# Kernel tuning notes

Measured on AMD Instinct MI355X. Metric: run time of the kernel, lower is better.

## Reference

```python
import jax, jax.numpy as jnp
from jax import lax
import numpy as np

# Dims matching init_kwargs
V = 32000      # vocab
D = 768        # d_model
L = 4          # n_layers
N = 16         # state_size
K = 4          # conv kernel
I = 2 * D      # intermediate = expand * d_model = 1536
DT = (D + 15) // 16  # time_step_rank = 48
BATCH, SEQ = 4, 2048
EPS = 1e-5


def setup_inputs() -> dict:
    key = jax.random.key(0)
    ks = jax.random.split(key, 12)
    s = 0.02
    A_init = jnp.broadcast_to(jnp.arange(1, N + 1, dtype=jnp.float32), (L, I, N))
    return {
        "input_ids": jax.random.randint(ks[0], (BATCH, SEQ), 0, V, dtype=jnp.int32),
        "embed": jax.random.normal(ks[1], (V, D), jnp.float32) * s,        # tied lm_head
        "norm_w": jnp.ones((L, D), jnp.float32),
        "in_proj_w": jax.random.normal(ks[2], (L, 2 * I, D), jnp.float32) * s,
        "conv_w": jax.random.normal(ks[3], (L, I, K), jnp.float32) * s,
        "conv_b": jnp.zeros((L, I), jnp.float32),
        "x_proj_w": jax.random.normal(ks[4], (L, DT + 2 * N, I), jnp.float32) * s,
        "dt_proj_w": jax.random.normal(ks[5], (L, I, DT), jnp.float32) * s,
        "dt_proj_b": jax.random.normal(ks[6], (L, I), jnp.float32) * s,
        "A_log": jnp.log(A_init),
        "D_param": jnp.ones((L, I), jnp.float32),
        "out_proj_w": jax.random.normal(ks[7], (L, D, I), jnp.float32) * s,
        "norm_f_w": jnp.ones((D,), jnp.float32),
    }


def rmsnorm(x, w):
    return x * lax.rsqrt(jnp.mean(x * x, axis=-1, keepdims=True) + EPS) * w


def mamba_mixer(x, in_w, cw, cb, xp_w, dtp_w, dtp_b, a_log, d_par, out_w):
    # x: [B, S, D]
    proj = jnp.einsum('bsd,ed->bse', x, in_w)            # [B, S, 2I]
    u, gate = jnp.split(proj, 2, axis=-1)                # each [B, S, I]
    # causal depthwise conv1d (HF pads K-1 then truncates to S == left pad)
    uc = u.transpose(0, 2, 1)                            # [B, I, S]
    conv = lax.conv_general_dilated(
        uc, cw[:, None, :], window_strides=(1,), padding=[(K - 1, 0)],
        feature_group_count=I, dimension_numbers=('NCH', 'OIH', 'NCH'))
    ut = jax.nn.silu(conv + cb[None, :, None]).transpose(0, 2, 1)  # [B, S, I]
    # SSM parameters
    xdbl = jnp.einsum('bsi,ei->bse', ut, xp_w)           # [B, S, DT+2N]
    dt_r = xdbl[..., :DT]
    Bm = xdbl[..., DT:DT + N]                            # [B, S, N]
    Cm = xdbl[..., DT + N:]                              # [B, S, N]
    dt = jax.nn.softplus(jnp.einsum('bsr,ir->bsi', dt_r, dtp_w) + dtp_b)  # [B, S, I]
    A = -jnp.exp(a_log)                                  # [I, N]

    def step(h, ins):
        dt_t, B_t, C_t, u_t = ins                        # [B,I],[B,N],[B,N],[B,I]
        dA = jnp.exp(dt_t[..., None] * A)                # [B, I, N]
        h = dA * h + (dt_t[..., None] * B_t[:, None, :]) * u_t[..., None]
        y = jnp.einsum('bin,bn->bi', h, C_t)
        return h, y

    h0 = jnp.zeros((x.shape[0], I, N), x.dtype)
    xs = (dt.transpose(1, 0, 2), Bm.transpose(1, 0, 2),
          Cm.transpose(1, 0, 2), ut.transpose(1, 0, 2))
    _, ys = lax.scan(step, h0, xs)                       # [S, B, I]
    y = ys.transpose(1, 0, 2) + ut * d_par               # skip D term
    y = y * jax.nn.silu(gate)
    return jnp.einsum('bsi,di->bsd', y, out_w)           # [B, S, D]


def reference(input_ids, embed, norm_w, in_proj_w, conv_w, conv_b, x_proj_w,
              dt_proj_w, dt_proj_b, A_log, D_param, out_proj_w, norm_f_w):
    h = embed[input_ids]                                 # [B, S, D]
    for l in range(L):
        h = h + mamba_mixer(rmsnorm(h, norm_w[l]), in_proj_w[l], conv_w[l],
                            conv_b[l], x_proj_w[l], dt_proj_w[l], dt_proj_b[l],
                            A_log[l], D_param[l], out_proj_w[l])
    h = rmsnorm(h, norm_f_w)
    # module returns logits[:, -1]; compute only last-token logits (tied lm_head)
    return h[:, -1] @ embed.T                            # [B, V]
```

## Files before the change

kernel.cpp:

```cpp
#include <hip/hip_runtime.h>
#include <hip/hip_bf16.h>

#define Vv 32000
#define Dm 768
#define Lm 4
#define Nst 16
#define Kc 4
#define Im 1536
#define DTr 48
#define Bt 4
#define Sq 2048
#define TOK (Bt*Sq)
#define EPSf 1e-5f
#define NC 64
#define CL 32
#define QROWS (Bt*NC*16)
#define LOG2E 1.4426950408889634f
#define LN2f  0.6931471805599453f

using bf16 = __hip_bfloat16;
typedef __bf16 bf16x8 __attribute__((ext_vector_type(8)));
typedef float f32x4 __attribute__((ext_vector_type(4)));

__device__ __forceinline__ float b2f(bf16 x){ return __bfloat162float(x); }
__device__ __forceinline__ bf16 f2b(float x){ return __float2bfloat16(x); }
__device__ __forceinline__ float us2f(ushort u){ unsigned x = (unsigned)u << 16; return __builtin_bit_cast(float, x); }

__device__ __forceinline__ float ex2(float x){
#if __has_builtin(__builtin_amdgcn_exp2f)
  return __builtin_amdgcn_exp2f(x);
#else
  float r; asm("v_exp_f32 %0, %1" : "=v"(r) : "v"(x)); return r;
#endif
}
__device__ __forceinline__ float vlog2(float x){
#if __has_builtin(__builtin_amdgcn_logf)
  return __builtin_amdgcn_logf(x);
#else
  float r; asm("v_log_f32 %0, %1" : "=v"(r) : "v"(x)); return r;
#endif
}
__device__ __forceinline__ float frcp(float x){
#if __has_builtin(__builtin_amdgcn_rcpf)
  return __builtin_amdgcn_rcpf(x);
#else
  float r; asm("v_rcp_f32 %0, %1" : "=v"(r) : "v"(x)); return r;
#endif
}

#define GLDS(gp, lp) __builtin_amdgcn_global_load_lds( \
    (const __attribute__((address_space(1))) void*)(gp), \
    (__attribute__((address_space(3))) void*)(lp), 16, 0, 0)

__global__ __launch_bounds__(256) void k_cvt(const float* __restrict__ src,
                                             bf16* __restrict__ dst, int n){
  int i = (blockIdx.x*256 + threadIdx.x)*4;
  if (i >= n) return;
  float4 v = *(const float4*)(src + i);
  bf16* o = dst + i;
  o[0]=f2b(v.x); o[1]=f2b(v.y); o[2]=f2b(v.z); o[3]=f2b(v.w);
}

__global__ __launch_bounds__(256) void k_cvt_xpw(const float* __restrict__ src,
                                                 bf16* __restrict__ dst){
  int idx = blockIdx.x*256 + threadIdx.x;
  int l = idx / (128*Im); int rem = idx - l*128*Im;
  int r = rem / Im;       int c = rem - r*Im;
  dst[idx] = (r < 80) ? f2b(src[((size_t)l*80 + r)*Im + c]) : f2b(0.f);
}

__global__ __launch_bounds__(256) void k_cvt_dtw(const float* __restrict__ src,
                                                 bf16* __restrict__ dst){
  int idx = blockIdx.x*256 + threadIdx.x;
  int l = idx / (Im*64); int rem = idx - l*Im*64;
  int r = rem / 64;      int c = rem - r*64;
  dst[idx] = (c < 48) ? f2b(src[((size_t)l*Im + r)*48 + c]) : f2b(0.f);
}

__global__ __launch_bounds__(256) void k_embed(const int* __restrict__ ids,
                                               const float* __restrict__ emb,
                                               float* __restrict__ h){
  int t = blockIdx.x;
  const float4* e = (const float4*)(emb + (size_t)ids[t]*Dm);
  float4* o = (float4*)(h + (size_t)t*Dm);
  if (threadIdx.x < Dm/4) o[threadIdx.x] = e[threadIdx.x];
}

__global__ __launch_bounds__(256) void k_rmsnorm(const float* __restrict__ h,
                                                 const float* __restrict__ w,
                                                 bf16* __restrict__ xb){
  int t = blockIdx.x;
  const float* x = h + (size_t)t*Dm;
  float v[3]; float ss = 0.f;
  #pragma unroll
  for (int j=0;j<3;j++){ v[j] = x[threadIdx.x + j*256]; ss += v[j]*v[j]; }
  #pragma unroll
  for (int off=32; off; off>>=1) ss += __shfl_xor(ss, off);
  __shared__ float sred[4];
  int wave = threadIdx.x>>6, lane = threadIdx.x&63;
  if (lane==0) sred[wave]=ss;
  __syncthreads();
  float tot = sred[0]+sred[1]+sred[2]+sred[3];
  float scale = rsqrtf(tot*(1.f/Dm) + EPSf);
  bf16* o = xb + (size_t)t*Dm;
  #pragma unroll
  for (int j=0;j<3;j++){ int d = threadIdx.x + j*256; o[d] = f2b(v[j]*scale*w[d]); }
}

__global__ __launch_bounds__(256) void k_rms_last(const float* __restrict__ h,
                                                  const float* __restrict__ w,
                                                  float* __restrict__ xf){
  int b = blockIdx.x;
  const float* x = h + ((size_t)b*Sq + (Sq-1))*Dm;
  float v[3]; float ss = 0.f;
  #pragma unroll
  for (int j=0;j<3;j++){ v[j] = x[threadIdx.x + j*256]; ss += v[j]*v[j]; }
  #pragma unroll
  for (int off=32; off; off>>=1) ss += __shfl_xor(ss, off);
  __shared__ float sred[4];
  int wave = threadIdx.x>>6, lane = threadIdx.x&63;
  if (lane==0) sred[wave]=ss;
  __syncthreads();
  float tot = sred[0]+sred[1]+sred[2]+sred[3];
  float scale = rsqrtf(tot*(1.f/Dm) + EPSf);
  float* o = xf + (size_t)b*Dm;
  #pragma unroll
  for (int j=0;j<3;j++){ int d = threadIdx.x + j*256; o[d] = v[j]*scale*w[d]; }
}

template<int MODE>
__global__ __launch_bounds__(256) void k_gemm(const bf16* __restrict__ A,
                                              const bf16* __restrict__ Bw,
                                              void* __restrict__ Cout,
                                              const float* __restrict__ bias,
                                              int M, int N, int K,
                                              int lda, int ldb, int ldc){
  __shared__ __align__(16) ushort Ash[128*32];
  __shared__ __align__(16) ushort Bsh[128*32];
  int tid = threadIdx.x;
  int bm = blockIdx.y, bn = blockIdx.x;
  int wave = tid >> 6, lane = tid & 63;
  int wrow = wave >> 1, wcol = wave & 1;
  int quad = lane >> 4, lq = lane & 15;

  f32x4 acc[4][4];
  #pragma unroll
  for (int a=0;a<4;a++)
    #pragma unroll
    for (int b=0;b<4;b++) acc[a][b] = (f32x4){0.f,0.f,0.f,0.f};

  const ushort* Ag = (const ushort*)A;
  const ushort* Bg = (const ushort*)Bw;

  for (int k0 = 0; k0 < K; k0 += 32) {
    __syncthreads();
    #pragma unroll
    for (int c = tid; c < 512; c += 256) {
      int row = c >> 2, col = (c & 3) * 8;
      GLDS(&Ag[(size_t)(bm*128 + row)*lda + k0 + col], &Ash[c*8]);
      GLDS(&Bg[(size_t)(bn*128 + row)*ldb + k0 + col], &Bsh[c*8]);
    }
    __syncthreads();
    bf16x8 af[4], bfr[4];
    #pragma unroll
    for (int a=0;a<4;a++){
      int m = wrow*64 + a*16 + lq;
      af[a] = __builtin_bit_cast(bf16x8, *(const uint4*)&Ash[m*32 + quad*8]);
    }
    #pragma unroll
    for (int b=0;b<4;b++){
      int n = wcol*64 + b*16 + lq;
      bfr[b] = __builtin_bit_cast(bf16x8, *(const uint4*)&Bsh[n*32 + quad*8]);
    }
    #pragma unroll
    for (int a=0;a<4;a++)
      #pragma unroll
      for (int b=0;b<4;b++)
        acc[a][b] = __builtin_amdgcn_mfma_f32_16x16x32_bf16(af[a], bfr[b], acc[a][b], 0, 0, 0);
  }
  #pragma unroll
  for (int a=0;a<4;a++)
    #pragma unroll
    for (int b=0;b<4;b++)
      #pragma unroll
      for (int r=0;r<4;r++){
        int row = bm*128 + wrow*64 + a*16 + quad*4 + r;
        int col = bn*128 + wcol*64 + b*16 + lq;
        size_t idx = (size_t)row*ldc + col;
        if (MODE == 0) ((bf16*)Cout)[idx] = f2b(acc[a][b][r]);
        else if (MODE == 1) ((float*)Cout)[idx] += acc[a][b][r];
        else {
          float v = acc[a][b][r] + bias[col];
          float sp;
          if (v > 20.f) sp = v;
          else { float e = ex2(v*LOG2E); sp = vlog2(1.f + e)*LN2f; }
          ((bf16*)Cout)[idx] = f2b(sp);
        }
      }
}

#define SA256(qm,k0s,bf_) { GLDS(Ag + sA[qm][0] + (k0s), lds + (bf_)*32768 + lA[qm][0]); \
                            GLDS(Ag + sA[qm][1] + (k0s), lds + (bf_)*32768 + lA[qm][1]); }
#define SB256(qn,k0s,bf_) { GLDS(Bg + sB[qn][0] + (k0s), lds + 65536 + (bf_)*32768 + lB[qn][0]); \
                            GLDS(Bg + sB[qn][1] + (k0s), lds + 65536 + (bf_)*32768 + lB[qn][1]); }
#define RD_A(qm_) do{ _Pragma("unroll") for(int m2=0;m2<4;m2++){ \
    int r = wm*128 + ((qm_)*4+m2)*16 + lq; \
    _Pragma("unroll") for(int kh=0;kh<2;kh++) \
      bA[m2][kh] = *(const uint4*)(Ab + (r<<7) + ((kh*64 + quad*16) ^ ((r&7)<<4))); } }while(0)
#define RD_B(qn_) do{ _Pragma("unroll") for(int n2=0;n2<2;n2++){ \
    int r = wn*64 + ((qn_)*2+n2)*16 + lq; \
    _Pragma("unroll") for(int kh=0;kh<2;kh++) \
      bB[qn_][n2][kh] = *(const uint4*)(Bb + (r<<7) + ((kh*64 + quad*16) ^ ((r&7)<<4))); } }while(0)
#define MMA256(qm_,qn_) do{ \
  __builtin_amdgcn_s_barrier(); \
  __builtin_amdgcn_sched_barrier(0); \
  __builtin_amdgcn_s_setprio(1); \
  _Pragma("unroll") for(int m2=0;m2<4;m2++) \
    _Pragma("unroll") for(int n2=0;n2<2;n2++) \
      _Pragma("unroll") for(int kh=0;kh<2;kh++) \
        acc[(qm_)*4+m2][(qn_)*2+n2] = __builtin_amdgcn_mfma_f32_16x16x32_bf16( \
          __builtin_bit_cast(bf16x8, bA[m2][kh]), __builtin_bit_cast(bf16x8, bB[qn_][n2][kh]), \
          acc[(qm_)*4+m2][(qn_)*2+n2], 0, 0, 0); \
  __builtin_amdgcn_s_setprio(0); \
  __builtin_amdgcn_s_barrier(); \
  __builtin_amdgcn_sched_barrier(0); \
}while(0)
#define VMW4 asm volatile("s_waitcnt vmcnt(4)":::"memory")

template<int MODE>
__global__ __launch_bounds__(512, 2) void k_gemm256(const bf16* __restrict__ A,
                                                    const bf16* __restrict__ Bw,
                                                    void* __restrict__ Cout,
                                                    int M, int N, int K,
                                                    int lda, int ldb, int ldc){
  __shared__ __align__(16) char lds[131072];
  int tid = threadIdx.x;
  int wave = tid >> 6, lane = tid & 63;
  int wm = wave >> 2, wn = wave & 3;
  int quad = lane >> 4, lq = lane & 15;
  int nx = gridDim.x;
  int nwg = nx * gridDim.y;
  int lin = blockIdx.y * nx + blockIdx.x;
  if ((nwg & 7) == 0){
    int cpx = nwg >> 3;
    lin = (lin & 7)*cpx + (lin >> 3);
  }
  int bm = lin / nx, bn = lin - bm*nx;
  const ushort* Ag = (const ushort*)A;
  const ushort* Bg = (const ushort*)Bw;

  size_t sA[2][2]; int lA[2][2];
  size_t sB[2][2]; int lB[2][2];
  #pragma unroll
  for (int qm=0; qm<2; qm++)
    #pragma unroll
    for (int d=0; d<2; d++){
      int r = d*128 + qm*64 + (tid>>3);
      int cb = ((tid&7)<<4) ^ ((r&7)<<4);
      sA[qm][d] = (size_t)(bm*256 + r)*lda + (cb>>1);
      lA[qm][d] = ((d*128 + qm*64)<<7) + tid*16;
    }
  #pragma unroll
  for (int qn=0; qn<2; qn++)
    #pragma unroll
    for (int d=0; d<2; d++){
      int g = 2*d + (wave>>2);
      int jj = tid & 255;
      int r = g*64 + qn*32 + (jj>>3);
      int cb = ((jj&7)<<4) ^ ((r&7)<<4);
      sB[qn][d] = (size_t)(bn*256 + r)*ldb + (cb>>1);
      lB[qn][d] = ((g*64 + qn*32)<<7) + jj*16;
    }

  f32x4 acc[8][4];
  #pragma unroll
  for (int a=0;a<8;a++)
    #pragma unroll
    for (int b=0;b<4;b++) acc[a][b] = (f32x4){0.f,0.f,0.f,0.f};

  SA256(0, 0, 0); SB256(0, 0, 0); SB256(1, 0, 0); SA256(1, 0, 0);
  VMW4;
  __builtin_amdgcn_s_barrier();
  __builtin_amdgcn_sched_barrier(0);

  uint4 bA[4][2], bB[2][2][2];
  int NT = K >> 6;
  for (int t = 0; t < NT-1; t++){
    int buf = t & 1, bufn = buf ^ 1;
    int k0n = (t+1) << 6;
    const char* Ab = lds + buf*32768;
    const char* Bb = lds + 65536 + buf*32768;
    RD_A(0); RD_B(0); SA256(0,k0n,bufn); VMW4; MMA256(0,0);
    RD_B(1);          SB256(0,k0n,bufn); VMW4; MMA256(0,1);
    RD_A(1);          SB256(1,k0n,bufn);       MMA256(1,0);
                      SA256(1,k0n,bufn); VMW4; MMA256(1,1);
  }
  {
    int buf = (NT-1) & 1;
    const char* Ab = lds + buf*32768;
    const char* Bb = lds + 65536 + buf*32768;
    RD_A(0); RD_B(0); asm volatile("s_waitcnt vmcnt(2)":::"memory"); MMA256(0,0);
    RD_B(1);          asm volatile("s_waitcnt vmcnt(0)":::"memory"); MMA256(0,1);
    RD_A(1);                                                          MMA256(1,0);
                                                                      MMA256(1,1);
  }

  #pragma unroll
  for (int mr=0; mr<8; mr++)
    #pragma unroll
    for (int nr=0; nr<4; nr++)
      #pragma unroll
      for (int rr=0; rr<4; rr++){
        int row = bm*256 + wm*128 + mr*16 + quad*4 + rr;
        int col = bn*256 + wn*64 + nr*16 + lq;
        size_t idx = (size_t)row*ldc + col;
        if (MODE == 0) ((bf16*)Cout)[idx] = f2b(acc[mr][nr][rr]);
        else ((float*)Cout)[idx] += acc[mr][nr][rr];
      }
}

__global__ __launch_bounds__(256) void k_conv(const bf16* __restrict__ proj,
                                              const float* __restrict__ cw,
                                              const float* __restrict__ cb,
                                              bf16* __restrict__ ut){
  int t = blockIdx.y;
  int i = blockIdx.x*256 + threadIdx.x;
  int s = t & (Sq-1);
  float acc = cb[i];
  #pragma unroll
  for (int k=0;k<Kc;k++){
    int sk = s + k - 3;
    if (sk >= 0) acc += b2f(proj[(size_t)(t+k-3)*(2*Im) + i]) * cw[i*Kc+k];
  }
  float sig = frcp(1.f + ex2(-acc*LOG2E));
  ut[(size_t)t*Im + i] = f2b(acc*sig);
}


__global__ __launch_bounds__(256) void k_scan1(const bf16* __restrict__ dt,
                                               const bf16* __restrict__ ut,
                                               const bf16* __restrict__ xdbl,
                                               const float* __restrict__ alog,
                                               bf16* __restrict__ Qb,
                                               float* __restrict__ S){
  __shared__ float s_b[CL][16];
  int tid = threadIdx.x;
  int i = blockIdx.x*256 + tid;
  int b = blockIdx.y, c = blockIdx.z;
  size_t tok0 = (size_t)b*Sq + c*CL;
  {
    int row = tid >> 1, part = tid & 1;
    if (row < CL){
      uint4 v = *(const uint4*)((const ushort*)xdbl + (tok0+row)*128 + 48 + part*8);
      const ushort* u = (const ushort*)&v;
      #pragma unroll
      for (int j=0;j<8;j++) s_b[row][part*8+j] = us2f(u[j]);
    }
  }
  float kn[16];
  {
    const float4* ap = (const float4*)(alog + (size_t)i*16);
    #pragma unroll
    for (int q=0;q<4;q++){
      float4 a4 = ap[q];
      kn[q*4+0] = -__expf(a4.x)*LOG2E; kn[q*4+1] = -__expf(a4.y)*LOG2E;
      kn[q*4+2] = -__expf(a4.z)*LOG2E; kn[q*4+3] = -__expf(a4.w)*LOG2E;
    }
  }
  bool fastp = true;
  #pragma unroll
  for (int n=1;n<16;n++)
    fastp = fastp && (fabsf(kn[n] - (float)(n+1)*kn[0]) <= 1e-4f*fabsf(kn[n]));
  __syncthreads();
  float h[16];
  #pragma unroll
  for (int n=0;n<16;n++) h[n]=0.f;
  float sum = 0.f;
  const ushort* dtp = (const ushort*)dt + tok0*Im + i;
  const ushort* utp = (const ushort*)ut + tok0*Im + i;
  ushort dA = dtp[0], uA = utp[0];
  ushort dB = dtp[Im], uB = utp[Im];
  if (fastp){
    float k0 = kn[0];
    for (int t = 0; t < CL; t++){
      float dtv = us2f(dA); float uv = us2f(uA);
      dA = dB; uA = uB;
      if (t+2 < CL){
        dB = dtp[(size_t)(t+2)*Im];
        uB = utp[(size_t)(t+2)*Im];
      }
      sum += dtv;
      float cdu = dtv*uv;
      const f32x4* brow = (const f32x4*)&s_b[t][0];
      f32x4 B0=brow[0], B1=brow[1], B2=brow[2], B3=brow[3];
      float Bv[16] = {B0[0],B0[1],B0[2],B0[3],B1[0],B1[1],B1[2],B1[3],
                      B2[0],B2[1],B2[2],B2[3],B3[0],B3[1],B3[2],B3[3]};
      float p1 = ex2(k0*dtv);
      float p2=p1*p1, p3=p2*p1, p4=p2*p2;
      float p5=p4*p1, p6=p4*p2, p7=p4*p3, p8=p4*p4;
      float d[16] = {p1,p2,p3,p4,p5,p6,p7,p8,
                     p8*p1,p8*p2,p8*p3,p8*p4,p8*p5,p8*p6,p8*p7,p8*p8};
      #pragma unroll
      for (int n=0;n<16;n++)
        h[n] = d[n]*h[n] + cdu*Bv[n];
    }
  } else {
    for (int t = 0; t < CL; t++){
      float dtv = us2f(dA); float uv = us2f(uA);
      dA = dB; uA = uB;
      if (t+2 < CL){
        dB = dtp[(size_t)(t+2)*Im];
        uB = utp[(size_t)(t+2)*Im];
      }
      sum += dtv;
      float cdu = dtv*uv;
      const f32x4* brow = (const f32x4*)&s_b[t][0];
      f32x4 B0=brow[0], B1=brow[1], B2=brow[2], B3=brow[3];
      float Bv[16] = {B0[0],B0[1],B0[2],B0[3],B1[0],B1[1],B1[2],B1[3],
                      B2[0],B2[1],B2[2],B2[3],B3[0],B3[1],B3[2],B3[3]};
      #pragma unroll
      for (int n=0;n<16;n++)
        h[n] = ex2(kn[n]*dtv)*h[n] + cdu*Bv[n];
    }
  }
  int rq = (b*NC + c)*16;
  S[(size_t)(b*NC + c)*Im + i] = sum;
  #pragma unroll
  for (int n=0;n<16;n++)
    Qb[(size_t)(rq+n)*2*Im + i] = f2b(h[n]);
}

__global__ __launch_bounds__(256) void k_scan2(const bf16* __restrict__ Qb,
                                               const float* __restrict__ S,
                                               const float* __restrict__ alog,
                                               bf16* __restrict__ Hinb){
  int idx = blockIdx.x*256 + threadIdx.x;
  int i = idx % Im; int bn = idx / Im;
  int n = bn & 15, b = bn >> 4;
  float kn = -__expf(alog[(size_t)i*16 + n])*LOG2E;
  float h = 0.f;
  for (int c = 0; c < NC; c++){
    size_t r = (size_t)((b*NC + c)*16 + n);
    Hinb[(QROWS + r)*2*Im + i] = f2b(h);
    float P = ex2(kn * S[(size_t)(b*NC + c)*Im + i]);
    h = P*h + b2f(Qb[r*2*Im + i]);
  }
}

__global__ __launch_bounds__(256) void k_scan3(const bf16* __restrict__ dt,
                                               const bf16* __restrict__ ut,
                                               const bf16* __restrict__ xdbl,
                                               const bf16* __restrict__ proj,
                                               const float* __restrict__ alog,
                                               const float* __restrict__ dpar,
                                               const bf16* __restrict__ Hinb,
                                               bf16* __restrict__ y){
  __shared__ float s_bc[CL][32];
  int tid = threadIdx.x;
  int i = blockIdx.x*256 + tid;
  int b = blockIdx.y, c = blockIdx.z;
  size_t tok0 = (size_t)b*Sq + c*CL;
  {
    int row = tid >> 1, part = tid & 1;
    if (row < CL){
      const ushort* src = (const ushort*)xdbl + (tok0+row)*128 + 48 + part*16;
      uint4 v0 = *(const uint4*)src;
      uint4 v1 = *(const uint4*)(src + 8);
      const ushort* u0 = (const ushort*)&v0;
      const ushort* u1 = (const ushort*)&v1;
      #pragma unroll
      for (int j=0;j<8;j++){
        s_bc[row][part*16 + j]     = us2f(u0[j]);
        s_bc[row][part*16 + 8 + j] = us2f(u1[j]);
      }
    }
  }
  float kn[16];
  {
    const float4* ap = (const float4*)(alog + (size_t)i*16);
    #pragma unroll
    for (int q=0;q<4;q++){
      float4 a4 = ap[q];
      kn[q*4+0] = -__expf(a4.x)*LOG2E; kn[q*4+1] = -__expf(a4.y)*LOG2E;
      kn[q*4+2] = -__expf(a4.z)*LOG2E; kn[q*4+3] = -__expf(a4.w)*LOG2E;
    }
  }
  bool fastp = true;
  #pragma unroll
  for (int n=1;n<16;n++)
    fastp = fastp && (fabsf(kn[n] - (float)(n+1)*kn[0]) <= 1e-4f*fabsf(kn[n]));
  float Dp = dpar[i];
  float h[16];
  {
    int rq = QROWS + (b*NC + c)*16;
    #pragma unroll
    for (int n=0;n<16;n++)
      h[n] = b2f(Hinb[(size_t)(rq+n)*2*Im + i]);
  }
  __syncthreads();
  const ushort* dtp = (const ushort*)dt + tok0*Im + i;
  const ushort* utp = (const ushort*)ut + tok0*Im + i;
  const ushort* gp  = (const ushort*)proj + tok0*2*Im + Im + i;
  ushort dA = dtp[0], uA = utp[0], gA = gp[0];
  ushort dB = dtp[Im], uB = utp[Im], gB = gp[2*Im];
  if (fastp){
    float k0 = kn[0];
    for (int t = 0; t < CL; t++){
      float dtv = us2f(dA); float uv = us2f(uA); float g = us2f(gA);
      dA = dB; uA = uB; gA = gB;
      if (t+2 < CL){
        dB = dtp[(size_t)(t+2)*Im];
        uB = utp[(size_t)(t+2)*Im];
        gB = gp[(size_t)(t+2)*2*Im];
      }
      float cdu = dtv*uv;
      const f32x4* brow = (const f32x4*)&s_bc[t][0];
      f32x4 B0=brow[0], B1=brow[1], B2=brow[2], B3=brow[3];
      f32x4 C0=brow[4], C1=brow[5], C2=brow[6], C3=brow[7];
      float Bv[16] = {B0[0],B0[1],B0[2],B0[3],B1[0],B1[1],B1[2],B1[3],
                      B2[0],B2[1],B2[2],B2[3],B3[0],B3[1],B3[2],B3[3]};
      float Cv[16] = {C0[0],C0[1],C0[2],C0[3],C1[0],C1[1],C1[2],C1[3],
                      C2[0],C2[1],C2[2],C2[3],C3[0],C3[1],C3[2],C3[3]};
      float p1 = ex2(k0*dtv);
      float p2=p1*p1, p3=p2*p1, p4=p2*p2;
      float p5=p4*p1, p6=p4*p2, p7=p4*p3, p8=p4*p4;
      float d[16] = {p1,p2,p3,p4,p5,p6,p7,p8,
                     p8*p1,p8*p2,p8*p3,p8*p4,p8*p5,p8*p6,p8*p7,p8*p8};
      float yv = 0.f;
      #pragma unroll
      for (int n=0;n<16;n++){
        h[n] = d[n]*h[n] + cdu*Bv[n];
        yv += h[n]*Cv[n];
      }
      float sig = frcp(1.f + ex2(-g*LOG2E));
      float outv = (yv + uv*Dp) * (g*sig);
      y[(tok0+t)*Im + i] = f2b(outv);
    }
  } else {
    for (int t = 0; t < CL; t++){
      float dtv = us2f(dA); float uv = us2f(uA); float g = us2f(gA);
      dA = dB; uA = uB; gA = gB;
      if (t+2 < CL){
        dB = dtp[(size_t)(t+2)*Im];
        uB = utp[(size_t)(t+2)*Im];
        gB = gp[(size_t)(t+2)*2*Im];
      }
      float cdu = dtv*uv;
      const f32x4* brow = (const f32x4*)&s_bc[t][0];
      f32x4 B0=brow[0], B1=brow[1], B2=brow[2], B3=brow[3];
      f32x4 C0=brow[4], C1=brow[5], C2=brow[6], C3=brow[7];
      float Bv[16] = {B0[0],B0[1],B0[2],B0[3],B1[0],B1[1],B1[2],B1[3],
                      B2[0],B2[1],B2[2],B2[3],B3[0],B3[1],B3[2],B3[3]};
      float Cv[16] = {C0[0],C0[1],C0[2],C0[3],C1[0],C1[1],C1[2],C1[3],
                      C2[0],C2[1],C2[2],C2[3],C3[0],C3[1],C3[2],C3[3]};
      float yv = 0.f;
      #pragma unroll
      for (int n=0;n<16;n++){
        h[n] = ex2(kn[n]*dtv)*h[n] + cdu*Bv[n];
        yv += h[n]*Cv[n];
      }
      float sig = frcp(1.f + ex2(-g*LOG2E));
      float outv = (yv + uv*Dp) * (g*sig);
      y[(tok0+t)*Im + i] = f2b(outv);
    }
  }
}

__global__ __launch_bounds__(256) void k_logits(const float* __restrict__ xf,
                                                const float* __restrict__ emb,
                                                float* __restrict__ out){
  __shared__ __align__(16) float xs[Bt*Dm];
  for (int j = threadIdx.x; j < Bt*Dm; j += 256) xs[j] = xf[j];
  __syncthreads();
  int wave = threadIdx.x>>6, lane = threadIdx.x&63;
  int v = blockIdx.x*4 + wave;
  const float4* e4 = (const float4*)(emb + (size_t)v*Dm);
  float a0=0.f,a1=0.f,a2=0.f,a3=0.f;
  for (int j = lane; j < Dm/4; j += 64){
    float4 ev = e4[j];
    float4 x0 = *(const float4*)&xs[j*4];
    float4 x1 = *(const float4*)&xs[Dm + j*4];
    float4 x2 = *(const float4*)&xs[2*Dm + j*4];
    float4 x3 = *(const float4*)&xs[3*Dm + j*4];
    a0 += ev.x*x0.x + ev.y*x0.y + ev.z*x0.z + ev.w*x0.w;
    a1 += ev.x*x1.x + ev.y*x1.y + ev.z*x1.z + ev.w*x1.w;
    a2 += ev.x*x2.x + ev.y*x2.y + ev.z*x2.z + ev.w*x2.w;
    a3 += ev.x*x3.x + ev.y*x3.y + ev.z*x3.z + ev.w*x3.w;
  }
  #pragma unroll
  for (int off=32; off; off>>=1){
    a0+=__shfl_xor(a0,off); a1+=__shfl_xor(a1,off);
    a2+=__shfl_xor(a2,off); a3+=__shfl_xor(a3,off);
  }
  if (lane==0){
    out[v]        = a0;
    out[Vv+v]     = a1;
    out[2*Vv+v]   = a2;
    out[3*Vv+v]   = a3;
  }
}

extern "C" void kernel_launch(void* const* d_in, const int* in_sizes, int n_in,
                              void* d_out, int out_size, void* d_ws, size_t ws_size,
                              hipStream_t stream){
  const int*   ids   = (const int*)d_in[0];
  const float* emb   = (const float*)d_in[1];
  const float* normw = (const float*)d_in[2];
  const float* inw   = (const float*)d_in[3];
  const float* cw    = (const float*)d_in[4];
  const float* cb    = (const float*)d_in[5];
  const float* xpw   = (const float*)d_in[6];
  const float* dtw   = (const float*)d_in[7];
  const float* dtb   = (const float*)d_in[8];
  const float* alog  = (const float*)d_in[9];
  const float* dpar  = (const float*)d_in[10];
  const float* outw  = (const float*)d_in[11];
  const float* normf = (const float*)d_in[12];
  float* out = (float*)d_out;

  char* p = (char*)d_ws;
  float* h    = (float*)p;  p += (size_t)TOK*Dm*4;
  bf16*  xb   = (bf16*)p;   p += (size_t)TOK*Dm*2;
  bf16*  proj = (bf16*)p;   p += (size_t)TOK*2*Im*2;
  bf16*  utb  = (bf16*)p;   p += (size_t)TOK*Im*2;
  bf16*  xdbl = (bf16*)p;   p += (size_t)TOK*128*2;
  bf16*  dtq  = (bf16*)p;   p += (size_t)TOK*Im*2;
  bf16*  yb   = (bf16*)p;   p += (size_t)TOK*Im*2;
  float* xf   = (float*)p;  p += (size_t)Bt*Dm*4;
  bf16*  inwb = (bf16*)p;   p += (size_t)Lm*2*Im*Dm*2;
  bf16*  outwb= (bf16*)p;   p += (size_t)Lm*Dm*Im*2;
  bf16*  xpwb = (bf16*)p;   p += (size_t)Lm*128*Im*2;
  bf16*  dtwb = (bf16*)p;   p += (size_t)Lm*Im*64*2;
  float* S = (float*)xb;

  { int n = Lm*2*Im*Dm; k_cvt<<<n/1024, 256, 0, stream>>>(inw, inwb, n); }
  { int n = Lm*Dm*Im;   k_cvt<<<n/1024, 256, 0, stream>>>(outw, outwb, n); }
  k_cvt_xpw<<<(Lm*128*Im)/256, 256, 0, stream>>>(xpw, xpwb);
  k_cvt_dtw<<<(Lm*Im*64)/256, 256, 0, stream>>>(dtw, dtwb);

  k_embed<<<TOK, 256, 0, stream>>>(ids, emb, h);

  for (int l = 0; l < Lm; l++){
    k_rmsnorm<<<TOK, 256, 0, stream>>>(h, normw + l*Dm, xb);
    k_gemm256<0><<<dim3((2*Im)/256, TOK/256), 512, 0, stream>>>(
        xb, inwb + (size_t)l*2*Im*Dm, proj, TOK, 2*Im, Dm, Dm, Dm, 2*Im);
    k_conv<<<dim3(Im/256, TOK), 256, 0, stream>>>(
        proj, cw + (size_t)l*Im*Kc, cb + (size_t)l*Im, utb);
    k_gemm<0><<<dim3(1, TOK/128), 256, 0, stream>>>(
        utb, xpwb + (size_t)l*128*Im, xdbl, nullptr, TOK, 128, Im, Im, Im, 128);
    k_gemm<3><<<dim3(Im/128, TOK/128), 256, 0, stream>>>(
        xdbl, dtwb + (size_t)l*Im*64, dtq, dtb + (size_t)l*Im, TOK, Im, 64, 128, 64, Im);
    k_scan1<<<dim3(Im/256, Bt, NC), 256, 0, stream>>>(
        dtq, utb, xdbl, alog + (size_t)l*Im*Nst, proj, S);
    k_scan2<<<(Bt*Nst*Im)/256, 256, 0, stream>>>(
        proj, S, alog + (size_t)l*Im*Nst, proj);
    k_scan3<<<dim3(Im/256, Bt, NC), 256, 0, stream>>>(
        dtq, utb, xdbl, proj, alog + (size_t)l*Im*Nst, dpar + (size_t)l*Im, proj, yb);
    k_gemm256<1><<<dim3(Dm/256, TOK/256), 512, 0, stream>>>(
        yb, outwb + (size_t)l*Dm*Im, h, TOK, Dm, Im, Im, Im, Dm);
  }

  k_rms_last<<<Bt, 256, 0, stream>>>(h, normf, xf);
  k_logits<<<Vv/4, 256, 0, stream>>>(xf, emb, out);
}
```

Baseline: 1.520 ms.

## Vectorize scan recurrences with packed float2 math and use 128-tile out-proj GEMM

```diff
diff --git a/kernel.cpp b/kernel.cpp
--- a/kernel.cpp
+++ b/kernel.cpp
@@ -21,6 +21,7 @@
 using bf16 = __hip_bfloat16;
 typedef __bf16 bf16x8 __attribute__((ext_vector_type(8)));
 typedef float f32x4 __attribute__((ext_vector_type(4)));
+typedef float f32x2 __attribute__((ext_vector_type(2)));
 
 __device__ __forceinline__ float b2f(bf16 x){ return __bfloat162float(x); }
 __device__ __forceinline__ bf16 f2b(float x){ return __float2bfloat16(x); }
@@ -372,16 +373,17 @@
   for (int n=1;n<16;n++)
     fastp = fastp && (fabsf(kn[n] - (float)(n+1)*kn[0]) <= 1e-4f*fabsf(kn[n]));
   __syncthreads();
-  float h[16];
-  #pragma unroll
-  for (int n=0;n<16;n++) h[n]=0.f;
   float sum = 0.f;
   const ushort* dtp = (const ushort*)dt + tok0*Im + i;
   const ushort* utp = (const ushort*)ut + tok0*Im + i;
   ushort dA = dtp[0], uA = utp[0];
   ushort dB = dtp[Im], uB = utp[Im];
+  int rq = (b*NC + c)*16;
   if (fastp){
     float k0 = kn[0];
+    f32x2 h2[8];
+    #pragma unroll
+    for (int j=0;j<8;j++) h2[j] = (f32x2){0.f,0.f};
     for (int t = 0; t < CL; t++){
       float dtv = us2f(dA); float uv = us2f(uA);
       dA = dB; uA = uB;
@@ -391,20 +393,36 @@
       }
       sum += dtv;
       float cdu = dtv*uv;
+      f32x2 cdu2 = (f32x2){cdu, cdu};
       const f32x4* brow = (const f32x4*)&s_b[t][0];
       f32x4 B0=brow[0], B1=brow[1], B2=brow[2], B3=brow[3];
-      float Bv[16] = {B0[0],B0[1],B0[2],B0[3],B1[0],B1[1],B1[2],B1[3],
-                      B2[0],B2[1],B2[2],B2[3],B3[0],B3[1],B3[2],B3[3]};
+      f32x2 Bv2[8] = {
+        __builtin_shufflevector(B0,B0,0,1), __builtin_shufflevector(B0,B0,2,3),
+        __builtin_shufflevector(B1,B1,0,1), __builtin_shufflevector(B1,B1,2,3),
+        __builtin_shufflevector(B2,B2,0,1), __builtin_shufflevector(B2,B2,2,3),
+        __builtin_shufflevector(B3,B3,0,1), __builtin_shufflevector(B3,B3,2,3)};
       float p1 = ex2(k0*dtv);
-      float p2=p1*p1, p3=p2*p1, p4=p2*p2;
-      float p5=p4*p1, p6=p4*p2, p7=p4*p3, p8=p4*p4;
-      float d[16] = {p1,p2,p3,p4,p5,p6,p7,p8,
-                     p8*p1,p8*p2,p8*p3,p8*p4,p8*p5,p8*p6,p8*p7,p8*p8};
-      #pragma unroll
-      for (int n=0;n<16;n++)
-        h[n] = d[n]*h[n] + cdu*Bv[n];
-    }
+      float p2 = p1*p1;
+      f32x2 d2[8];
+      d2[0] = (f32x2){p1,p2};
+      f32x2 pp = (f32x2){p2,p2};
+      d2[1] = d2[0]*pp;
+      pp = (f32x2){d2[1][1], d2[1][1]};
+      d2[2] = d2[0]*pp;
+      d2[3] = d2[1]*pp;
+      pp = (f32x2){d2[3][1], d2[3][1]};
+      d2[4]=d2[0]*pp; d2[5]=d2[1]*pp; d2[6]=d2[2]*pp; d2[7]=d2[3]*pp;
+      #pragma unroll
+      for (int j=0;j<8;j++)
+        h2[j] = d2[j]*h2[j] + cdu2*Bv2[j];
+    }
+    #pragma unroll
+    for (int n=0;n<16;n++)
+      Qb[(size_t)(rq+n)*2*Im + i] = f2b(h2[n>>1][n&1]);
   } else {
+    float h[16];
+    #pragma unroll
+    for (int n=0;n<16;n++) h[n]=0.f;
     for (int t = 0; t < CL; t++){
       float dtv = us2f(dA); float uv = us2f(uA);
       dA = dB; uA = uB;
@@ -422,12 +440,11 @@
       for (int n=0;n<16;n++)
         h[n] = ex2(kn[n]*dtv)*h[n] + cdu*Bv[n];
     }
-  }
-  int rq = (b*NC + c)*16;
+    #pragma unroll
+    for (int n=0;n<16;n++)
+      Qb[(size_t)(rq+n)*2*Im + i] = f2b(h[n]);
+  }
   S[(size_t)(b*NC + c)*Im + i] = sum;
-  #pragma unroll
-  for (int n=0;n<16;n++)
-    Qb[(size_t)(rq+n)*2*Im + i] = f2b(h[n]);
 }
 
 __global__ __launch_bounds__(256) void k_scan2(const bf16* __restrict__ Qb,
@@ -490,13 +507,7 @@
   for (int n=1;n<16;n++)
     fastp = fastp && (fabsf(kn[n] - (float)(n+1)*kn[0]) <= 1e-4f*fabsf(kn[n]));
   float Dp = dpar[i];
-  float h[16];
-  {
-    int rq = QROWS + (b*NC + c)*16;
-    #pragma unroll
-    for (int n=0;n<16;n++)
-      h[n] = b2f(Hinb[(size_t)(rq+n)*2*Im + i]);
-  }
+  int rq = QROWS + (b*NC + c)*16;
   __syncthreads();
   const ushort* dtp = (const ushort*)dt + tok0*Im + i;
   const ushort* utp = (const ushort*)ut + tok0*Im + i;
@@ -505,6 +516,11 @@
   ushort dB = dtp[Im], uB = utp[Im], gB = gp[2*Im];
   if (fastp){
     float k0 = kn[0];
+    f32x2 h2[8];
+    #pragma unroll
+    for (int j=0;j<8;j++)
+      h2[j] = (f32x2){ b2f(Hinb[(size_t)(rq+2*j)*2*Im + i]),
+                       b2f(Hinb[(size_t)(rq+2*j+1)*2*Im + i]) };
     for (int t = 0; t < CL; t++){
       float dtv = us2f(dA); float uv = us2f(uA); float g = us2f(gA);
       dA = dB; uA = uB; gA = gB;
@@ -514,29 +530,47 @@
         gB = gp[(size_t)(t+2)*2*Im];
       }
       float cdu = dtv*uv;
+      f32x2 cdu2 = (f32x2){cdu, cdu};
       const f32x4* brow = (const f32x4*)&s_bc[t][0];
       f32x4 B0=brow[0], B1=brow[1], B2=brow[2], B3=brow[3];
       f32x4 C0=brow[4], C1=brow[5], C2=brow[6], C3=brow[7];
-      float Bv[16] = {B0[0],B0[1],B0[2],B0[3],B1[0],B1[1],B1[2],B1[3],
-                      B2[0],B2[1],B2[2],B2[3],B3[0],B3[1],B3[2],B3[3]};
-      float Cv[16] = {C0[0],C0[1],C0[2],C0[3],C1[0],C1[1],C1[2],C1[3],
-                      C2[0],C2[1],C2[2],C2[3],C3[0],C3[1],C3[2],C3[3]};
+      f32x2 Bv2[8] = {
+        __builtin_shufflevector(B0,B0,0,1), __builtin_shufflevector(B0,B0,2,3),
+        __builtin_shufflevector(B1,B1,0,1), __builtin_shufflevector(B1,B1,2,3),
+        __builtin_shufflevector(B2,B2,0,1), __builtin_shufflevector(B2,B2,2,3),
+        __builtin_shufflevector(B3,B3,0,1), __builtin_shufflevector(B3,B3,2,3)};
+      f32x2 Cv2[8] = {
+        __builtin_shufflevector(C0,C0,0,1), __builtin_shufflevector(C0,C0,2,3),
+        __builtin_shufflevector(C1,C1,0,1), __builtin_shufflevector(C1,C1,2,3),
+        __builtin_shufflevector(C2,C2,0,1), __builtin_shufflevector(C2,C2,2,3),
+        __builtin_shufflevector(C3,C3,0,1), __builtin_shufflevector(C3,C3,2,3)};
       float p1 = ex2(k0*dtv);
-      float p2=p1*p1, p3=p2*p1, p4=p2*p2;
-      float p5=p4*p1, p6=p4*p2, p7=p4*p3, p8=p4*p4;
-      float d[16] = {p1,p2,p3,p4,p5,p6,p7,p8,
-                     p8*p1,p8*p2,p8*p3,p8*p4,p8*p5,p8*p6,p8*p7,p8*p8};
-      float yv = 0.f;
-      #pragma unroll
-      for (int n=0;n<16;n++){
-        h[n] = d[n]*h[n] + cdu*Bv[n];
-        yv += h[n]*Cv[n];
-      }
+      float p2 = p1*p1;
+      f32x2 d2[8];
+      d2[0] = (f32x2){p1,p2};
+      f32x2 pp = (f32x2){p2,p2};
+      d2[1] = d2[0]*pp;
+      pp = (f32x2){d2[1][1], d2[1][1]};
+      d2[2] = d2[0]*pp;
+      d2[3] = d2[1]*pp;
+      pp = (f32x2){d2[3][1], d2[3][1]};
+      d2[4]=d2[0]*pp; d2[5]=d2[1]*pp; d2[6]=d2[2]*pp; d2[7]=d2[3]*pp;
+      f32x2 yv2 = (f32x2){0.f, 0.f};
+      #pragma unroll
+      for (int j=0;j<8;j++){
+        h2[j] = d2[j]*h2[j] + cdu2*Bv2[j];
+        yv2 = yv2 + h2[j]*Cv2[j];
+      }
+      float yv = yv2[0] + yv2[1];
       float sig = frcp(1.f + ex2(-g*LOG2E));
       float outv = (yv + uv*Dp) * (g*sig);
       y[(tok0+t)*Im + i] = f2b(outv);
     }
   } else {
+    float h[16];
+    #pragma unroll
+    for (int n=0;n<16;n++)
+      h[n] = b2f(Hinb[(size_t)(rq+n)*2*Im + i]);
     for (int t = 0; t < CL; t++){
       float dtv = us2f(dA); float uv = us2f(uA); float g = us2f(gA);
       dA = dB; uA = uB; gA = gB;
@@ -656,8 +690,8 @@
         proj, S, alog + (size_t)l*Im*Nst, proj);
     k_scan3<<<dim3(Im/256, Bt, NC), 256, 0, stream>>>(
         dtq, utb, xdbl, proj, alog + (size_t)l*Im*Nst, dpar + (size_t)l*Im, proj, yb);
-    k_gemm256<1><<<dim3(Dm/256, TOK/256), 512, 0, stream>>>(
-        yb, outwb + (size_t)l*Dm*Im, h, TOK, Dm, Im, Im, Im, Dm);
+    k_gemm<1><<<dim3(Dm/128, TOK/128), 256, 0, stream>>>(
+        yb, outwb + (size_t)l*Dm*Im, h, nullptr, TOK, Dm, Im, Im, Im, Dm);
   }
 
   k_rms_last<<<Bt, 256, 0, stream>>>(h, normf, xf);
```

Result: faster. 1.357 ms (-10.7%).
